# Kernel tuning notes

Hardware: AMD Instinct MI355X
Metric: run time of the kernel (lower is better)

Reference implementation:

```python
import jax, jax.numpy as jnp
import numpy as np

N_HEADS = 8
D_HEAD = 64
INNER = N_HEADS * D_HEAD  # 512
D_X = 512
D_CTX = 768

def setup_inputs() -> dict:
    key = jax.random.key(0)
    ks = jax.random.split(key, 7)
    x = jax.random.normal(ks[0], (4, 4096, D_X), dtype=jnp.float32)
    context = jax.random.normal(ks[1], (4, 1024, D_CTX), dtype=jnp.float32)
    # Glorot-ish scaled params
    Wq = jax.random.normal(ks[2], (D_X, INNER), dtype=jnp.float32) / np.sqrt(D_X)
    Wk = jax.random.normal(ks[3], (D_CTX, INNER), dtype=jnp.float32) / np.sqrt(D_CTX)
    Wv = jax.random.normal(ks[4], (D_CTX, INNER), dtype=jnp.float32) / np.sqrt(D_CTX)
    Wo = jax.random.normal(ks[5], (INNER, INNER), dtype=jnp.float32) / np.sqrt(INNER)
    bo = jnp.zeros((INNER,), dtype=jnp.float32)
    return {"x": x, "context": context, "Wq": Wq, "Wk": Wk, "Wv": Wv, "Wo": Wo, "bo": bo}

def reference(x, context, Wq, Wk, Wv, Wo, bo):
    B, Nq, _ = x.shape
    Nc = context.shape[1]
    scale = D_HEAD ** -0.5
    # QKV projections (no bias), reshape to heads: b s (h d) -> b h s d
    q = (x @ Wq).reshape(B, Nq, N_HEADS, D_HEAD).transpose(0, 2, 1, 3)
    k = (context @ Wk).reshape(B, Nc, N_HEADS, D_HEAD).transpose(0, 2, 1, 3)
    v = (context @ Wv).reshape(B, Nc, N_HEADS, D_HEAD).transpose(0, 2, 1, 3)
    # scores: [B, H, Nq, Nc]
    score = jnp.einsum('bhqd,bhkd->bhqk', q, k) * scale
    weights = jax.nn.softmax(score, axis=-1)
    attn = jnp.einsum('bhqk,bhkd->bhqd', weights, v)
    out = attn.transpose(0, 2, 1, 3).reshape(B, Nq, INNER)
    return out @ Wo + bo
```

## Files before the change

### kernel.cpp

```cpp
#include <hip/hip_runtime.h>
#include <math.h>

typedef __attribute__((ext_vector_type(8))) short s8v;
typedef __attribute__((ext_vector_type(4))) float f4v;
typedef unsigned short u16;
typedef unsigned int u32;

constexpr int Bsz = 4, NQ = 4096, NC = 1024, NH = 8, DH = 64, DI = 512, DC = 768;

__device__ __forceinline__ u16 f2bf(float f) {
  union { float f; u32 u; } v; v.f = f;
  u32 r = v.u + 0x7fff + ((v.u >> 16) & 1);
  return (u16)(r >> 16);
}

__device__ __forceinline__ u32 pack2(float a, float b) {
  union { float f; u32 u; } ua, ub; ua.f = a; ub.f = b;
#if __has_builtin(__builtin_amdgcn_perm)
  return __builtin_amdgcn_perm(ub.u + 0x8000u, ua.u + 0x8000u, 0x07060302u);
#else
  return ((ub.u + 0x8000u) & 0xffff0000u) | ((ua.u + 0x8000u) >> 16);
#endif
}

#if __has_builtin(__builtin_amdgcn_exp2f)
#define EXP2(x) __builtin_amdgcn_exp2f(x)
#else
#define EXP2(x) exp2f(x)
#endif

__device__ __forceinline__ void g2l16(const void* g, void* l) {
  __builtin_amdgcn_global_load_lds((const __attribute__((address_space(1))) u32*)g,
                                   (__attribute__((address_space(3))) u32*)l, 16, 0, 0);
}

__global__ __launch_bounds__(256) void prep(const float* __restrict__ x, const float* __restrict__ ctx,
                                            const float* __restrict__ Wq, const float* __restrict__ Wk,
                                            const float* __restrict__ Wv, const float* __restrict__ Wo,
                                            u16* __restrict__ xb, u16* __restrict__ cb,
                                            u16* __restrict__ wqT, u16* __restrict__ wkvT,
                                            u16* __restrict__ woT) {
  int bx = blockIdx.x;
  if (bx < 11264) {
    const int NX4 = Bsz * NQ * DI / 4;
    const int NC4 = Bsz * NC * DC / 4;
    int i = bx * 256 + threadIdx.x;
    float4 v; u16* dst; int j;
    if (i < NX4) { v = ((const float4*)x)[i]; dst = xb; j = i; }
    else { j = i - NX4; if (j >= NC4) return; v = ((const float4*)ctx)[j]; dst = cb; }
    ushort4 o; o.x = f2bf(v.x); o.y = f2bf(v.y); o.z = f2bf(v.z); o.w = f2bf(v.w);
    ((ushort4*)dst)[j] = o;
    return;
  }
  int idx = bx - 11264;
  int z = idx / 96, rem = idx % 96, kx = rem % 12, ny = rem / 12;
  const float* src; u16* dst; int K; const int N = 512;
  if (z == 0)      { src = Wq; dst = wqT;              K = 512; }
  else if (z == 1) { src = Wk; dst = wkvT;             K = 768; }
  else if (z == 2) { src = Wv; dst = wkvT + 512 * 768; K = 768; }
  else             { src = Wo; dst = woT;              K = 512; }
  int k0 = kx * 64, n0 = ny * 64;
  if (k0 >= K) return;
  __shared__ u16 t[64][65];
  int tid = threadIdx.x, jr = tid & 63, ir = tid >> 6;
  for (int it = 0; it < 16; ++it) { int i = it * 4 + ir; t[i][jr] = f2bf(src[(size_t)(k0 + i) * N + n0 + jr]); }
  __syncthreads();
  for (int it = 0; it < 16; ++it) { int i = it * 4 + ir; dst[(size_t)(n0 + i) * K + k0 + jr] = t[jr][i]; }
}

template <int MODE>
__device__ __forceinline__ void gemm_body(const u16* __restrict__ A, const u16* __restrict__ Bt,
                                          void* __restrict__ C0, void* __restrict__ C1,
                                          const float* __restrict__ bias, int N, int K,
                                          float oscale, int nbx, int mby,
                                          u16* Al, u16* Bl) {
  int mb = mby * 128, nb = nbx * 128;
  int tid = threadIdx.x, lane = tid & 63, quad = lane >> 4, l16 = lane & 15, wave = tid >> 6;
  int wm = (wave >> 1) * 64, wn = (wave & 1) * 64;
  f4v acc[4][4];
  #pragma unroll
  for (int i = 0; i < 4; i++)
    #pragma unroll
    for (int j = 0; j < 4; j++) acc[i][j] = (f4v){0.f, 0.f, 0.f, 0.f};

  int r0 = tid >> 2, c0 = (tid & 3) * 8;
  const u16* Ap0 = A + (size_t)(mb + r0) * K + c0;
  const u16* Ap1 = A + (size_t)(mb + r0 + 64) * K + c0;
  const u16* Bp0 = Bt + (size_t)(nb + r0) * K + c0;
  const u16* Bp1 = Bt + (size_t)(nb + r0 + 64) * K + c0;

#define GSTAGE(k0, buf) do { \
    u16* al_ = Al + (buf) * 4096; u16* bl_ = Bl + (buf) * 4096; \
    g2l16(Ap0 + (k0), al_ + tid * 8); \
    g2l16(Ap1 + (k0), al_ + (tid + 256) * 8); \
    g2l16(Bp0 + (k0), bl_ + tid * 8); \
    g2l16(Bp1 + (k0), bl_ + (tid + 256) * 8); } while (0)

  GSTAGE(0, 0);
  int nk = K >> 5;
  for (int t = 0; t < nk; ++t) {
    __syncthreads();
    if (t + 1 < nk) GSTAGE((t + 1) * 32, (t + 1) & 1);
    const u16* al = Al + (t & 1) * 4096;
    const u16* bl = Bl + (t & 1) * 4096;
    s8v af[4], bfr[4];
    #pragma unroll
    for (int i = 0; i < 4; i++) af[i] = *(const s8v*)(al + (wm + i * 16 + l16) * 32 + quad * 8);
    #pragma unroll
    for (int j = 0; j < 4; j++) bfr[j] = *(const s8v*)(bl + (wn + j * 16 + l16) * 32 + quad * 8);
    #pragma unroll
    for (int i = 0; i < 4; i++)
      #pragma unroll
      for (int j = 0; j < 4; j++)
        acc[i][j] = __builtin_amdgcn_mfma_f32_16x16x32_bf16(af[i], bfr[j], acc[i][j], 0, 0, 0);
  }
#undef GSTAGE
  #pragma unroll
  for (int i = 0; i < 4; i++) {
    int rbase = mb + wm + i * 16 + quad * 4;
    #pragma unroll
    for (int j = 0; j < 4; j++) {
      int col = nb + wn + j * 16 + l16;
      if (MODE == 0) {
        u16* Cb = (u16*)C0;
        #pragma unroll
        for (int r = 0; r < 4; r++) Cb[(size_t)(rbase + r) * N + col] = f2bf(acc[i][j][r] * oscale);
      } else if (MODE == 1) {
        float* Cf = (float*)C0;
        #pragma unroll
        for (int r = 0; r < 4; r++) Cf[(size_t)(rbase + r) * N + col] = acc[i][j][r] + bias[col];
      } else {
        if (col < 512) {
          u16* Kb = (u16*)C0;
          #pragma unroll
          for (int r = 0; r < 4; r++) Kb[(size_t)(rbase + r) * 512 + col] = f2bf(acc[i][j][r]);
        } else {
          u16* Vt = (u16*)C1;
          int hd = col - 512, h = hd >> 6, d = hd & 63;
          int bb = rbase >> 10, tl = rbase & 1023;
          int tbase = tl & ~63, a0 = tl & 63;
          int pb = (a0 & 32) + ((a0 & 15) >> 2) * 8 + (((a0 >> 4) & 1) << 2);
          uint2 ov;
          ov.x = pack2(acc[i][j][0], acc[i][j][1]);
          ov.y = pack2(acc[i][j][2], acc[i][j][3]);
          *(uint2*)(Vt + ((size_t)(bb * NH + h) * DH + d) * NC + tbase + pb) = ov;
        }
      }
    }
  }
}

__global__ __launch_bounds__(256, 3) void proj_all(const u16* __restrict__ xb, const u16* __restrict__ cb,
                                                   const u16* __restrict__ wqT, const u16* __restrict__ wkvT,
                                                   u16* __restrict__ Qb, u16* __restrict__ Kb,
                                                   u16* __restrict__ Vtb, float qscale) {
  __shared__ alignas(16) u16 Al[2][128][32];
  __shared__ alignas(16) u16 Bl[2][128][32];
  int bx = blockIdx.x;
  if (bx < 512) {
    gemm_body<0>(xb, wqT, Qb, nullptr, nullptr, 512, 512, qscale, bx & 3, bx >> 2,
                 (u16*)Al, (u16*)Bl);
  } else {
    int bi = bx - 512;
    gemm_body<2>(cb, wkvT, Kb, Vtb, nullptr, 1024, 768, 1.0f, bi & 7, bi >> 3,
                 (u16*)Al, (u16*)Bl);
  }
}

__global__ __launch_bounds__(256, 2) void outproj(const u16* __restrict__ Ob, const u16* __restrict__ woT,
                                                  float* __restrict__ out, const float* __restrict__ bo) {
  __shared__ alignas(16) u16 Al[2][128][32];
  __shared__ alignas(16) u16 Bl[2][128][32];
  gemm_body<1>(Ob, woT, out, nullptr, bo, 512, 512, 1.0f, blockIdx.x, blockIdx.y,
               (u16*)Al, (u16*)Bl);
}

__global__ __launch_bounds__(256, 4) void attn(const u16* __restrict__ Q, const u16* __restrict__ Kb,
                                               const u16* __restrict__ Vt, u16* __restrict__ O) {
  __shared__ alignas(16) u16 Kl[2][64][64];
  __shared__ alignas(16) u16 Vl[2][64][64];
  int qt = blockIdx.x, h = blockIdx.y, b = blockIdx.z;
  int tid = threadIdx.x, wave = tid >> 6, lane = tid & 63, quad = lane >> 4, l16 = lane & 15;
  int q0 = qt * 128 + wave * 32;
  int x7 = l16 & 7;

  int kr = tid >> 3, kc = (tid & 7) ^ (kr & 7);
  const u16* kg = Kb + ((size_t)b * NC + kr) * 512 + h * DH + kc * 8;
  const u16* vg = Vt + ((size_t)(b * NH + h) * DH + kr) * NC + kc * 8;

#define ASTAGE(kt, buf) do { \
    const u16* kg_ = kg + (size_t)(kt) * 64 * 512; \
    const u16* vg_ = vg + (kt) * 64; \
    u16* kl_ = (u16*)Kl + (buf) * 4096; u16* vl_ = (u16*)Vl + (buf) * 4096; \
    g2l16(kg_,            kl_ + tid * 8); \
    g2l16(kg_ + 32 * 512, kl_ + (tid + 256) * 8); \
    g2l16(vg_,            vl_ + tid * 8); \
    g2l16(vg_ + 32 * NC,  vl_ + (tid + 256) * 8); } while (0)

  s8v aq[2][2];
  {
    const u16* Qp = Q + ((size_t)b * NQ + q0 + l16) * DI + h * DH + quad * 8;
    #pragma unroll
    for (int n = 0; n < 2; n++) {
      aq[n][0] = *(const s8v*)(Qp + (size_t)n * 16 * DI);
      aq[n][1] = *(const s8v*)(Qp + (size_t)n * 16 * DI + 32);
    }
  }
  f4v oacc[4][2];
  float lsum[2] = {0.f, 0.f};
  #pragma unroll
  for (int d = 0; d < 4; d++)
    #pragma unroll
    for (int n = 0; n < 2; n++) oacc[d][n] = (f4v){0.f, 0.f, 0.f, 0.f};

  ASTAGE(0, 0);
  for (int kt = 0; kt < NC / 64; ++kt) {
    int buf = kt & 1;
    __syncthreads();
    if (kt + 1 < NC / 64) ASTAGE(kt + 1, buf ^ 1);
    const u16* kb = (const u16*)Kl + buf * 4096;
    const u16* vb = (const u16*)Vl + buf * 4096;

    #pragma unroll
    for (int c = 0; c < 2; c++) {
      f4v S[2][2];
      #pragma unroll
      for (int mi = 0; mi < 2; mi++)
        #pragma unroll
        for (int n = 0; n < 2; n++) S[mi][n] = (f4v){0.f, 0.f, 0.f, 0.f};
      #pragma unroll
      for (int cd = 0; cd < 2; cd++) {
        int rA = 32 * c + l16;
        int ch = ((4 * cd + quad) ^ x7) * 8;
        s8v kf0 = *(const s8v*)(kb + rA * 64 + ch);
        s8v kf1 = *(const s8v*)(kb + (rA + 16) * 64 + ch);
        #pragma unroll
        for (int n = 0; n < 2; n++) {
          S[0][n] = __builtin_amdgcn_mfma_f32_16x16x32_bf16(kf0, aq[n][cd], S[0][n], 0, 0, 0);
          S[1][n] = __builtin_amdgcn_mfma_f32_16x16x32_bf16(kf1, aq[n][cd], S[1][n], 0, 0, 0);
        }
      }
      s8v pf[2];
      #pragma unroll
      for (int n = 0; n < 2; n++) {
        float p00 = EXP2(S[0][n][0]), p01 = EXP2(S[0][n][1]), p02 = EXP2(S[0][n][2]), p03 = EXP2(S[0][n][3]);
        float p10 = EXP2(S[1][n][0]), p11 = EXP2(S[1][n][1]), p12 = EXP2(S[1][n][2]), p13 = EXP2(S[1][n][3]);
        lsum[n] += (p00 + p01) + (p02 + p03) + (p10 + p11) + (p12 + p13);
        union { u32 d[4]; s8v v; } u;
        u.d[0] = pack2(p00, p01); u.d[1] = pack2(p02, p03);
        u.d[2] = pack2(p10, p11); u.d[3] = pack2(p12, p13);
        pf[n] = u.v;
      }
      #pragma unroll
      for (int d = 0; d < 4; d++) {
        int rV = d * 16 + l16;
        int ch = ((4 * c + quad) ^ x7) * 8;
        s8v vf = *(const s8v*)(vb + rV * 64 + ch);
        #pragma unroll
        for (int n = 0; n < 2; n++)
          oacc[d][n] = __builtin_amdgcn_mfma_f32_16x16x32_bf16(vf, pf[n], oacc[d][n], 0, 0, 0);
      }
    }
  }
#undef ASTAGE

  float inv[2];
  #pragma unroll
  for (int n = 0; n < 2; n++) {
    float s = lsum[n];
    s += __shfl_xor(s, 16); s += __shfl_xor(s, 32);
    inv[n] = 1.0f / s;
  }
  #pragma unroll
  for (int d = 0; d < 4; d++)
    #pragma unroll
    for (int n = 0; n < 2; n++) {
      int q = q0 + n * 16 + l16;
      uint2 ov;
      ov.x = pack2(oacc[d][n][0] * inv[n], oacc[d][n][1] * inv[n]);
      ov.y = pack2(oacc[d][n][2] * inv[n], oacc[d][n][3] * inv[n]);
      *(uint2*)(O + ((size_t)b * NQ + q) * DI + h * DH + d * 16 + quad * 4) = ov;
    }
}

extern "C" void kernel_launch(void* const* d_in, const int* in_sizes, int n_in,
                              void* d_out, int out_size, void* d_ws, size_t ws_size,
                              hipStream_t stream) {
  const float* x   = (const float*)d_in[0];
  const float* ctx = (const float*)d_in[1];
  const float* Wq  = (const float*)d_in[2];
  const float* Wk  = (const float*)d_in[3];
  const float* Wv  = (const float*)d_in[4];
  const float* Wo  = (const float*)d_in[5];
  const float* bo  = (const float*)d_in[6];
  float* out = (float*)d_out;

  u16* w    = (u16*)d_ws;
  u16* xb   = w;
  u16* cb   = xb   + 8388608;
  u16* wqT  = cb   + 3145728;
  u16* wkvT = wqT  + 262144;
  u16* woT  = wkvT + 786432;
  u16* Qb   = woT  + 262144;
  u16* Kbuf = Qb   + 8388608;
  u16* Vtb  = Kbuf + 2097152;
  u16* Ob   = Vtb  + 2097152;

  const float qscale = 0.125f * 1.44269504f;

  prep<<<11648, 256, 0, stream>>>(x, ctx, Wq, Wk, Wv, Wo, xb, cb, wqT, wkvT, woT);
  proj_all<<<768, 256, 0, stream>>>(xb, cb, wqT, wkvT, Qb, Kbuf, Vtb, qscale);
  attn<<<dim3(32, 8, 4), 256, 0, stream>>>(Qb, Kbuf, Vtb, Ob);
  outproj<<<dim3(4, 128), 256, 0, stream>>>(Ob, woT, out, bo);
}
```

Baseline: 196.1 us.

## Restructure attention inner loop: MFMA row-sum, hardware bf16 pack, setprio interleaving

The two-chunk score loop is split so both score blocks are computed up front, with their exp/pack and PV stages issued separately under s_setprio hints. This lets MFMA work overlap with the transcendental VALU work. The softmax denominator is now accumulated with an MFMA against a ones vector instead of scalar adds plus cross-lane shuffles. Manual bf16 packing is replaced by the v_cvt_pk_bf16_f32 instruction. The changes lower VALU pressure at the cost of extra MFMAs and more live accumulator registers. The row-sum now uses bf16-rounded probabilities, which matches the values used in PV.

```diff
diff --git a/kernel.cpp b/kernel.cpp
--- a/kernel.cpp
+++ b/kernel.cpp
@@ -21,6 +21,12 @@
 #else
   return ((ub.u + 0x8000u) & 0xffff0000u) | ((ua.u + 0x8000u) >> 16);
 #endif
+}
+
+__device__ __forceinline__ u32 cvtpk(float a, float b) {
+  u32 r;
+  asm("v_cvt_pk_bf16_f32 %0, %1, %2" : "=v"(r) : "v"(a), "v"(b));
+  return r;
 }
 
 #if __has_builtin(__builtin_amdgcn_exp2f)
@@ -206,12 +212,18 @@
       aq[n][1] = *(const s8v*)(Qp + (size_t)n * 16 * DI + 32);
     }
   }
+  s8v vones;
+  #pragma unroll
+  for (int i = 0; i < 8; i++) vones[i] = (short)0x3F80;
+
   f4v oacc[4][2];
-  float lsum[2] = {0.f, 0.f};
+  f4v lacc[2];
   #pragma unroll
   for (int d = 0; d < 4; d++)
     #pragma unroll
     for (int n = 0; n < 2; n++) oacc[d][n] = (f4v){0.f, 0.f, 0.f, 0.f};
+  #pragma unroll
+  for (int n = 0; n < 2; n++) lacc[n] = (f4v){0.f, 0.f, 0.f, 0.f};
 
   ASTAGE(0, 0);
   for (int kt = 0; kt < NC / 64; ++kt) {
@@ -221,64 +233,94 @@
     const u16* kb = (const u16*)Kl + buf * 4096;
     const u16* vb = (const u16*)Vl + buf * 4096;
 
-    #pragma unroll
-    for (int c = 0; c < 2; c++) {
-      f4v S[2][2];
-      #pragma unroll
-      for (int mi = 0; mi < 2; mi++)
-        #pragma unroll
-        for (int n = 0; n < 2; n++) S[mi][n] = (f4v){0.f, 0.f, 0.f, 0.f};
-      #pragma unroll
-      for (int cd = 0; cd < 2; cd++) {
-        int rA = 32 * c + l16;
-        int ch = ((4 * cd + quad) ^ x7) * 8;
-        s8v kf0 = *(const s8v*)(kb + rA * 64 + ch);
-        s8v kf1 = *(const s8v*)(kb + (rA + 16) * 64 + ch);
-        #pragma unroll
-        for (int n = 0; n < 2; n++) {
-          S[0][n] = __builtin_amdgcn_mfma_f32_16x16x32_bf16(kf0, aq[n][cd], S[0][n], 0, 0, 0);
-          S[1][n] = __builtin_amdgcn_mfma_f32_16x16x32_bf16(kf1, aq[n][cd], S[1][n], 0, 0, 0);
-        }
+    f4v S0[2][2], S1[2][2];
+    #pragma unroll
+    for (int mi = 0; mi < 2; mi++)
+      #pragma unroll
+      for (int n = 0; n < 2; n++) { S0[mi][n] = (f4v){0.f,0.f,0.f,0.f}; S1[mi][n] = (f4v){0.f,0.f,0.f,0.f}; }
+    __builtin_amdgcn_s_setprio(1);
+    #pragma unroll
+    for (int cd = 0; cd < 2; cd++) {
+      int ch = ((4 * cd + quad) ^ x7) * 8;
+      s8v k00 = *(const s8v*)(kb + (l16     ) * 64 + ch);
+      s8v k01 = *(const s8v*)(kb + (l16 + 16) * 64 + ch);
+      #pragma unroll
+      for (int n = 0; n < 2; n++) {
+        S0[0][n] = __builtin_amdgcn_mfma_f32_16x16x32_bf16(k00, aq[n][cd], S0[0][n], 0, 0, 0);
+        S0[1][n] = __builtin_amdgcn_mfma_f32_16x16x32_bf16(k01, aq[n][cd], S0[1][n], 0, 0, 0);
       }
-      s8v pf[2];
+      s8v k10 = *(const s8v*)(kb + (l16 + 32) * 64 + ch);
+      s8v k11 = *(const s8v*)(kb + (l16 + 48) * 64 + ch);
       #pragma unroll
       for (int n = 0; n < 2; n++) {
-        float p00 = EXP2(S[0][n][0]), p01 = EXP2(S[0][n][1]), p02 = EXP2(S[0][n][2]), p03 = EXP2(S[0][n][3]);
-        float p10 = EXP2(S[1][n][0]), p11 = EXP2(S[1][n][1]), p12 = EXP2(S[1][n][2]), p13 = EXP2(S[1][n][3]);
-        lsum[n] += (p00 + p01) + (p02 + p03) + (p10 + p11) + (p12 + p13);
-        union { u32 d[4]; s8v v; } u;
-        u.d[0] = pack2(p00, p01); u.d[1] = pack2(p02, p03);
-        u.d[2] = pack2(p10, p11); u.d[3] = pack2(p12, p13);
-        pf[n] = u.v;
+        S1[0][n] = __builtin_amdgcn_mfma_f32_16x16x32_bf16(k10, aq[n][cd], S1[0][n], 0, 0, 0);
+        S1[1][n] = __builtin_amdgcn_mfma_f32_16x16x32_bf16(k11, aq[n][cd], S1[1][n], 0, 0, 0);
       }
-      #pragma unroll
-      for (int d = 0; d < 4; d++) {
-        int rV = d * 16 + l16;
-        int ch = ((4 * c + quad) ^ x7) * 8;
-        s8v vf = *(const s8v*)(vb + rV * 64 + ch);
-        #pragma unroll
-        for (int n = 0; n < 2; n++)
-          oacc[d][n] = __builtin_amdgcn_mfma_f32_16x16x32_bf16(vf, pf[n], oacc[d][n], 0, 0, 0);
-      }
-    }
+    }
+    __builtin_amdgcn_s_setprio(0);
+
+    s8v pf0[2];
+    #pragma unroll
+    for (int n = 0; n < 2; n++) {
+      float p00 = EXP2(S0[0][n][0]), p01 = EXP2(S0[0][n][1]), p02 = EXP2(S0[0][n][2]), p03 = EXP2(S0[0][n][3]);
+      float p10 = EXP2(S0[1][n][0]), p11 = EXP2(S0[1][n][1]), p12 = EXP2(S0[1][n][2]), p13 = EXP2(S0[1][n][3]);
+      union { u32 d[4]; s8v v; } u;
+      u.d[0] = cvtpk(p00, p01); u.d[1] = cvtpk(p02, p03);
+      u.d[2] = cvtpk(p10, p11); u.d[3] = cvtpk(p12, p13);
+      pf0[n] = u.v;
+    }
+    __builtin_amdgcn_s_setprio(1);
+    #pragma unroll
+    for (int n = 0; n < 2; n++)
+      lacc[n] = __builtin_amdgcn_mfma_f32_16x16x32_bf16(vones, pf0[n], lacc[n], 0, 0, 0);
+    #pragma unroll
+    for (int d = 0; d < 4; d++) {
+      int ch = (quad ^ x7) * 8;
+      s8v vf = *(const s8v*)(vb + (d * 16 + l16) * 64 + ch);
+      #pragma unroll
+      for (int n = 0; n < 2; n++)
+        oacc[d][n] = __builtin_amdgcn_mfma_f32_16x16x32_bf16(vf, pf0[n], oacc[d][n], 0, 0, 0);
+    }
+    __builtin_amdgcn_s_setprio(0);
+
+    s8v pf1[2];
+    #pragma unroll
+    for (int n = 0; n < 2; n++) {
+      float p00 = EXP2(S1[0][n][0]), p01 = EXP2(S1[0][n][1]), p02 = EXP2(S1[0][n][2]), p03 = EXP2(S1[0][n][3]);
+      float p10 = EXP2(S1[1][n][0]), p11 = EXP2(S1[1][n][1]), p12 = EXP2(S1[1][n][2]), p13 = EXP2(S1[1][n][3]);
+      union { u32 d[4]; s8v v; } u;
+      u.d[0] = cvtpk(p00, p01); u.d[1] = cvtpk(p02, p03);
+      u.d[2] = cvtpk(p10, p11); u.d[3] = cvtpk(p12, p13);
+      pf1[n] = u.v;
+    }
+    __builtin_amdgcn_s_setprio(1);
+    #pragma unroll
+    for (int n = 0; n < 2; n++)
+      lacc[n] = __builtin_amdgcn_mfma_f32_16x16x32_bf16(vones, pf1[n], lacc[n], 0, 0, 0);
+    #pragma unroll
+    for (int d = 0; d < 4; d++) {
+      int ch = ((4 + quad) ^ x7) * 8;
+      s8v vf = *(const s8v*)(vb + (d * 16 + l16) * 64 + ch);
+      #pragma unroll
+      for (int n = 0; n < 2; n++)
+        oacc[d][n] = __builtin_amdgcn_mfma_f32_16x16x32_bf16(vf, pf1[n], oacc[d][n], 0, 0, 0);
+    }
+    __builtin_amdgcn_s_setprio(0);
   }
 #undef ASTAGE
 
   float inv[2];
   #pragma unroll
-  for (int n = 0; n < 2; n++) {
-    float s = lsum[n];
-    s += __shfl_xor(s, 16); s += __shfl_xor(s, 32);
-    inv[n] = 1.0f / s;
-  }
+  for (int n = 0; n < 2; n++) inv[n] = 1.0f / lacc[n][0];
+
   #pragma unroll
   for (int d = 0; d < 4; d++)
     #pragma unroll
     for (int n = 0; n < 2; n++) {
       int q = q0 + n * 16 + l16;
       uint2 ov;
-      ov.x = pack2(oacc[d][n][0] * inv[n], oacc[d][n][1] * inv[n]);
-      ov.y = pack2(oacc[d][n][2] * inv[n], oacc[d][n][3] * inv[n]);
+      ov.x = cvtpk(oacc[d][n][0] * inv[n], oacc[d][n][1] * inv[n]);
+      ov.y = cvtpk(oacc[d][n][2] * inv[n], oacc[d][n][3] * inv[n]);
       *(uint2*)(O + ((size_t)b * NQ + q) * DI + h * DH + d * 16 + quad * 4) = ov;
     }
 }
```

Result: faster. 188.3 us (-4.0%).
